# Kernel tuning notes

Hardware: AMD Instinct MI355X
Metric: run time of the kernel (lower is better)

The kernel has to match this reference:

```python
import jax, jax.numpy as jnp
import numpy as np

B, S, N_IN, N_OUT = 4, 192, 256, 1

def setup_inputs() -> dict:
    key = jax.random.key(0)
    ks = jax.random.split(key, 7)
    scale = 1.0 / np.sqrt(N_IN)
    return {
        "h_head": jax.random.normal(ks[0], (B, S, N_IN), jnp.float32),
        "h_dep": jax.random.normal(ks[1], (B, S, N_IN), jnp.float32),
        "h_sib": jax.random.normal(ks[2], (B, S, N_IN), jnp.float32),
        "W_tri": jax.random.normal(ks[3], (N_OUT, N_IN, N_IN, N_IN), jnp.float32) * (scale / N_IN),
        "U_hd": jax.random.normal(ks[4], (N_OUT, N_IN, N_IN), jnp.float32) * scale,
        "V_hs": jax.random.normal(ks[5], (N_OUT, N_IN, N_IN), jnp.float32) * scale,
        "Z_ds": jax.random.normal(ks[6], (N_OUT, N_IN, N_IN), jnp.float32) * scale,
        "bias": jnp.zeros((N_OUT,), jnp.float32),
    }

def reference(h_head, h_dep, h_sib, W_tri, U_hd, V_hs, Z_ds, bias):
    # biaffine terms: [b, x, y, o]
    s_hd = jnp.einsum('bhi,oij,bdj->bhdo', h_head, U_hd, h_dep)
    s_hs = jnp.einsum('bhi,oij,bsj->bhso', h_head, V_hs, h_sib)
    s_ds = jnp.einsum('bdi,oij,bsj->bdso', h_dep, Z_ds, h_sib)
    # trilinear term: note j,k of W_tri appear nowhere else, so they are
    # reduced first (w_red[o,i] = sum_{j,k} W_tri[o,i,j,k]) — same math as
    # torch.einsum('bhi,bdi,bsi,oijk->bhdso', ...).
    w_red = jnp.sum(W_tri, axis=(2, 3))  # [o, i]
    s_tri = jnp.einsum('bhi,bdi,bsi,oi->bhdso', h_head, h_dep, h_sib, w_red)
    scores = (s_tri
              + s_hd[:, :, :, None, :]   # unsqueeze sib axis
              + s_hs[:, :, None, :, :]   # unsqueeze dep axis
              + s_ds[:, None, :, :, :]   # unsqueeze head axis
              + bias)
    return scores[..., 0]  # n_out == 1 -> squeeze last dim
```

## Files before the change

kernel.cpp:

```cpp
#include <hip/hip_runtime.h>
#include <stdint.h>

#define NB 4
#define SS 192
#define NI 256

typedef __attribute__((ext_vector_type(8))) short bf16x8;
typedef __attribute__((ext_vector_type(16))) float f32x16;

__device__ __forceinline__ uint16_t f2bf(float f) {
  union { float f; uint32_t u; } v; v.f = f;
  return (uint16_t)((v.u + 0x7FFFu + ((v.u >> 16) & 1u)) >> 16);
}

__device__ __forceinline__ uint4 pack8(const float4 a, const float4 b) {
  uint4 r;
  r.x = (uint32_t)f2bf(a.x) | ((uint32_t)f2bf(a.y) << 16);
  r.y = (uint32_t)f2bf(a.z) | ((uint32_t)f2bf(a.w) << 16);
  r.z = (uint32_t)f2bf(b.x) | ((uint32_t)f2bf(b.y) << 16);
  r.w = (uint32_t)f2bf(b.z) | ((uint32_t)f2bf(b.w) << 16);
  return r;
}

__device__ __forceinline__ uint32_t bfmul2(uint32_t x, uint32_t y) {
  union { float f; uint32_t u; } xa, xb, ya, yb, r0, r1;
  xa.u = x << 16;        ya.u = y << 16;
  xb.u = x & 0xFFFF0000u; yb.u = y & 0xFFFF0000u;
  r0.f = xa.f * ya.f;
  r1.f = xb.f * yb.f;
  uint32_t lo = (r0.u + 0x7FFFu + ((r0.u >> 16) & 1u)) >> 16;
  uint32_t hi = (r1.u + 0x7FFFu + ((r1.u >> 16) & 1u)) >> 16;
  return lo | (hi << 16);
}


__global__ __launch_bounds__(256) void kA(
    const float* __restrict__ W,
    const float* __restrict__ h_head, const float* __restrict__ h_dep, const float* __restrict__ h_sib,
    const float* __restrict__ U, const float* __restrict__ V, const float* __restrict__ Z,
    float* __restrict__ partial,
    uint16_t* __restrict__ HH, uint16_t* __restrict__ HD, uint16_t* __restrict__ HS,
    uint16_t* __restrict__ dU16, uint16_t* __restrict__ T216, uint16_t* __restrict__ TZ16) {
  const int bi = blockIdx.x, tid = threadIdx.x;

  if (bi >= 120) {
    __shared__ float red[4];
    const int c = bi - 120;
    const float4* pw = (const float4*)(W + (size_t)c * 8192);
    float4 a = {0.f, 0.f, 0.f, 0.f};
    #pragma unroll
    for (int it = 0; it < 8; ++it) {
      const float4 v = pw[it * 256 + tid];
      a.x += v.x; a.y += v.y; a.z += v.z; a.w += v.w;
    }
    float s = (a.x + a.y) + (a.z + a.w);
    for (int off = 32; off > 0; off >>= 1) s += __shfl_down(s, off, 64);
    if ((tid & 63) == 0) red[tid >> 6] = s;
    __syncthreads();
    if (tid == 0) partial[c] = red[0] + red[1] + red[2] + red[3];
    return;
  }
  if (bi >= 24) {
    const int rl = tid >> 5, c8 = tid & 31;
    const int g = (bi - 24) * 8 + rl;
    const int dst = g * 32 + (c8 ^ (g & 15));
    const int srci = g * 64 + c8 * 2;
    { const float4 x = ((const float4*)h_head)[srci], y = ((const float4*)h_head)[srci + 1];
      ((uint4*)HH)[dst] = pack8(x, y); }
    { const float4 x = ((const float4*)h_dep)[srci], y = ((const float4*)h_dep)[srci + 1];
      ((uint4*)HD)[dst] = pack8(x, y); }
    { const float4 x = ((const float4*)h_sib)[srci], y = ((const float4*)h_sib)[srci + 1];
      ((uint4*)HS)[dst] = pack8(x, y); }
    return;
  }

  {
    __shared__ __align__(16) uint16_t Ah[192 * 128];
    __shared__ __align__(16) uint16_t Bh[128 * 128];
    const int which = bi >> 3, rem = bi & 7;
    const int b = rem >> 1, nt = rem & 1;
    const float* As = (which == 0) ? h_dep : h_sib;
    const float* Bs = (which == 0) ? U : (which == 1) ? V : Z;
    uint16_t* Os = (which == 0) ? dU16 : (which == 1) ? T216 : TZ16;
    const int lane = tid & 63, w = tid >> 6;
    const int l31 = lane & 31, l5 = lane >> 5;
    const int N0 = nt * 128;
    f32x16 acc[6] = {};

    #pragma unroll
    for (int kh = 0; kh < 2; ++kh) {
      const int kbase = kh * 128;
      if (kh) __syncthreads();
      #pragma unroll
      for (int i = 0; i < 12; ++i) {
        const int slot = i * 256 + tid;
        const int row = slot >> 4, ck = slot & 15;
        const float* sp = As + (size_t)(b * SS + row) * NI + kbase + ck * 8;
        const float4 x = *(const float4*)sp, y = *(const float4*)(sp + 4);
        *(uint4*)((char*)Ah + row * 256 + ((ck ^ (row & 15)) << 4)) = pack8(x, y);
      }
      #pragma unroll
      for (int i = 0; i < 8; ++i) {
        const int slot = i * 256 + tid;
        const int row = slot >> 4, ck = slot & 15;
        const float* sp = Bs + (size_t)(N0 + row) * NI + kbase + ck * 8;
        const float4 x = *(const float4*)sp, y = *(const float4*)(sp + 4);
        *(uint4*)((char*)Bh + row * 256 + ((ck ^ (row & 15)) << 4)) = pack8(x, y);
      }
      __syncthreads();
      const int brow = w * 32 + l31;
      const int bbyte = brow * 256;
      const int bmask = brow & 15;
      #pragma unroll
      for (int ks = 0; ks < 8; ++ks) {
        const int sl = ks * 2 + l5;
        bf16x8 bf = *reinterpret_cast<const bf16x8*>((const char*)Bh + bbyte + ((sl ^ bmask) << 4));
        #pragma unroll
        for (int mt = 0; mt < 6; ++mt) {
          const int ar = mt * 32 + l31;
          bf16x8 af = *reinterpret_cast<const bf16x8*>((const char*)Ah + ar * 256 + ((sl ^ (ar & 15)) << 4));
          acc[mt] = __builtin_amdgcn_mfma_f32_32x32x16_bf16(af, bf, acc[mt], 0, 0, 0);
        }
      }
    }
    const int n = N0 + w * 32 + l31;
    const int nck = n >> 3, npos = n & 7;
    #pragma unroll
    for (int mt = 0; mt < 6; ++mt) {
      #pragma unroll
      for (int r = 0; r < 16; ++r) {
        const int m = mt * 32 + (r & 3) + 8 * (r >> 2) + 4 * l5;
        Os[(size_t)(b * SS + m) * NI + ((nck ^ (m & 15)) << 3) + npos] = f2bf(acc[mt][r]);
      }
    }
  }
}

__global__ __launch_bounds__(384, 1) void k_s2(
    const uint16_t* __restrict__ HH, const uint16_t* __restrict__ HD,
    const uint16_t* __restrict__ dU16, const uint16_t* __restrict__ T216, const uint16_t* __restrict__ TZ16,
    float* __restrict__ s_hd, float* __restrict__ s_hs, float* __restrict__ s_ds) {
  __shared__ __align__(16) uint16_t Ah[192 * 128];
  __shared__ __align__(16) uint16_t Bh[192 * 128];
  const int which = blockIdx.x, b = blockIdx.y;
  const uint16_t* As = (which == 2) ? HD : HH;
  const uint16_t* Bs = (which == 0) ? dU16 : (which == 1) ? T216 : TZ16;
  float* Os = (which == 0) ? s_hd : (which == 1) ? s_hs : s_ds;
  const int tid = threadIdx.x, lane = tid & 63, w = tid >> 6;
  const int l31 = lane & 31, l5 = lane >> 5;
  f32x16 acc[6] = {};

  #pragma unroll
  for (int kh = 0; kh < 2; ++kh) {
    const int kbase = kh * 128;
    if (kh) __syncthreads();
    #pragma unroll
    for (int i = 0; i < 8; ++i) {
      const int slot = i * 384 + tid;
      const int row = slot >> 4, ck = slot & 15;
      const uint16_t* src = As + (size_t)(b * SS + row) * NI + kbase + ck * 8;
      __builtin_amdgcn_global_load_lds((const __attribute__((address_space(1))) void*)src,
          (__attribute__((address_space(3))) void*)(Ah + (size_t)slot * 8), 16, 0, 0);
    }
    #pragma unroll
    for (int i = 0; i < 8; ++i) {
      const int slot = i * 384 + tid;
      const int row = slot >> 4, ck = slot & 15;
      const uint16_t* src = Bs + (size_t)(b * SS + row) * NI + kbase + ck * 8;
      __builtin_amdgcn_global_load_lds((const __attribute__((address_space(1))) void*)src,
          (__attribute__((address_space(3))) void*)(Bh + (size_t)slot * 8), 16, 0, 0);
    }
    __syncthreads();
    const int brow = w * 32 + l31;
    const int bbyte = brow * 256;
    const int bmask = brow & 15;
    #pragma unroll
    for (int ks = 0; ks < 8; ++ks) {
      const int sl = ks * 2 + l5;
      bf16x8 bf = *reinterpret_cast<const bf16x8*>((const char*)Bh + bbyte + ((sl ^ bmask) << 4));
      #pragma unroll
      for (int mt = 0; mt < 6; ++mt) {
        const int ar = mt * 32 + l31;
        bf16x8 af = *reinterpret_cast<const bf16x8*>((const char*)Ah + ar * 256 + ((sl ^ (ar & 15)) << 4));
        acc[mt] = __builtin_amdgcn_mfma_f32_32x32x16_bf16(af, bf, acc[mt], 0, 0, 0);
      }
    }
  }
  const int n = w * 32 + l31;
  #pragma unroll
  for (int mt = 0; mt < 6; ++mt) {
    #pragma unroll
    for (int r = 0; r < 16; ++r) {
      const int m = mt * 32 + (r & 3) + 8 * (r >> 2) + 4 * l5;
      Os[(size_t)(b * SS + m) * SS + n] = acc[mt][r];
    }
  }
}

__global__ __launch_bounds__(576) void k3_big(
    const uint16_t* __restrict__ HH, const uint16_t* __restrict__ HS,
    const float* __restrict__ h_dep, const float* __restrict__ partial,
    const float* __restrict__ s_hd, const float* __restrict__ s_hs,
    const float* __restrict__ s_ds,
    const float* __restrict__ bias, float* __restrict__ out) {
  __shared__ __align__(16) uint16_t Btile[96 * 128];
  __shared__ __align__(16) uint16_t Atile[96 * 128];
  __shared__ uint16_t cvec[NI];
  __shared__ float chd_s[96];
  const int d = blockIdx.x, hb = blockIdx.y >> 1, sb = blockIdx.y & 1, b = blockIdx.z;
  const int tid = threadIdx.x;
  const int lane = tid & 63, w = tid >> 6;
  const int wh = w / 3, ws = w % 3;
  const int l31 = lane & 31, l5 = lane >> 5;

  if (tid < NI) {
    float wr = 0.f;
    #pragma unroll
    for (int q = 0; q < 8; ++q) wr += partial[8 * tid + q];
    cvec[tid] = f2bf(wr * h_dep[(b * SS + d) * NI + tid]);
  } else if (tid < NI + 96) {
    const int t = tid - NI;
    chd_s[t] = s_hd[(size_t)(b * SS + hb * 96 + t) * SS + d];
  }
  __syncthreads();

  f32x16 acc = {};

  #pragma unroll
  for (int half = 0; half < 2; ++half) {
    const int kbase = half * 128;
    if (half) __syncthreads();
    #pragma unroll
    for (int i = 0; i < 3; ++i) {
      const int slot = i * 576 + tid;
      if (slot < 1536) {
        const int row = slot >> 4;
        const uint16_t* src = HS + ((size_t)(b * SS + sb * 96 + row) << 8) + kbase + (slot & 15) * 8;
        __builtin_amdgcn_global_load_lds(
            (const __attribute__((address_space(1))) void*)src,
            (__attribute__((address_space(3))) void*)(Btile + (size_t)slot * 8),
            16, 0, 0);
      }
    }
    #pragma unroll
    for (int i = 0; i < 3; ++i) {
      const int slot = i * 576 + tid;
      if (slot < 1536) {
        const int row = slot >> 4;
        const int kc = slot & 15;
        const int lcl = kc ^ (row & 15);
        const uint4 cv4 = *(const uint4*)(cvec + kbase + lcl * 8);
        const uint4 hh4 = *(const uint4*)(HH + ((size_t)(b * SS + hb * 96 + row) << 8) + kbase + kc * 8);
        uint4 a4;
        a4.x = bfmul2(hh4.x, cv4.x);
        a4.y = bfmul2(hh4.y, cv4.y);
        a4.z = bfmul2(hh4.z, cv4.z);
        a4.w = bfmul2(hh4.w, cv4.w);
        *(uint4*)((char*)Atile + (size_t)slot * 16) = a4;
      }
    }
    __syncthreads();
    const int arow = wh * 32 + l31;
    const int abyte = arow * 256;
    const int amask = arow & 15;
    const int brow = ws * 32 + l31;
    const int bbyte = brow * 256;
    const int bmask = brow & 15;
    #pragma unroll
    for (int ks = 0; ks < 8; ++ks) {
      const int sl = ks * 2 + l5;
      bf16x8 af = *reinterpret_cast<const bf16x8*>((const char*)Atile + abyte + ((sl ^ amask) << 4));
      bf16x8 bf = *reinterpret_cast<const bf16x8*>((const char*)Btile + bbyte + ((sl ^ bmask) << 4));
      acc = __builtin_amdgcn_mfma_f32_32x32x16_bf16(af, bf, acc, 0, 0, 0);
    }
  }

  const float bias0 = bias[0];
  const int s = sb * 96 + ws * 32 + l31;
  const float dsv = s_ds[(b * SS + d) * SS + s];
  #pragma unroll
  for (int r = 0; r < 16; ++r) {
    const int hl = wh * 32 + (r & 3) + 8 * (r >> 2) + 4 * l5;
    const float v = acc[r] + chd_s[hl] + bias0
                  + s_hs[(size_t)(b * SS + hb * 96 + hl) * SS + s] + dsv;
    out[((size_t)(b * SS + hb * 96 + hl) * SS + d) * SS + s] = v;
  }
}

extern "C" void kernel_launch(void* const* d_in, const int* in_sizes, int n_in,
                              void* d_out, int out_size, void* d_ws, size_t ws_size,
                              hipStream_t stream) {
  const float* h_head = (const float*)d_in[0];
  const float* h_dep  = (const float*)d_in[1];
  const float* h_sib  = (const float*)d_in[2];
  const float* W_tri  = (const float*)d_in[3];
  const float* U_hd   = (const float*)d_in[4];
  const float* V_hs   = (const float*)d_in[5];
  const float* Z_ds   = (const float*)d_in[6];
  const float* bias   = (const float*)d_in[7];
  float* out = (float*)d_out;

  float* ws = (float*)d_ws;
  float* partial = ws;          ws += 2048;
  float* s_hd    = ws;          ws += NB * SS * SS;
  float* s_hs    = ws;          ws += NB * SS * SS;
  float* s_ds    = ws;          ws += NB * SS * SS;
  uint16_t* HH   = (uint16_t*)ws;
  uint16_t* HD   = HH + NB * SS * NI;
  uint16_t* HS   = HD + NB * SS * NI;
  uint16_t* dU16 = HS + NB * SS * NI;
  uint16_t* T216 = dU16 + NB * SS * NI;
  uint16_t* TZ16 = T216 + NB * SS * NI;

  kA<<<2168, 256, 0, stream>>>(W_tri, h_head, h_dep, h_sib, U_hd, V_hs, Z_ds,
                               partial, HH, HD, HS, dU16, T216, TZ16);
  k_s2<<<dim3(3, NB), 384, 0, stream>>>(HH, HD, dU16, T216, TZ16, s_hd, s_hs, s_ds);
  k3_big<<<dim3(SS, 4, NB), 576, 0, stream>>>(HH, HS, h_dep, partial,
                                              s_hd, s_hs, s_ds, bias, out);
}
```

Measured before the change: 71.29 us.

## Widen k3_big tile to cover all sib positions per block

Each k3_big block now covers 96 head rows by all 192 sib positions with 384 threads, instead of 96x96 with 576 threads. Each wave holds three accumulators and reuses one A fragment across three MFMAs. The scaled A tile (head times cvec) is therefore built once per block, removing the duplicate construction across the two sib halves, and the grid has half as many blocks. In exchange the B tile doubles, raising LDS per block to roughly 72KB, which may cut how many blocks fit on a CU, and register pressure rises from the extra accumulators.

Result: slower. 73.61 us (+3.3%).

```diff
diff --git a/kernel.cpp b/kernel.cpp
--- a/kernel.cpp
+++ b/kernel.cpp
@@ -197,20 +197,21 @@
   }
 }
 
-__global__ __launch_bounds__(576) void k3_big(
+__global__ __launch_bounds__(384, 3) void k3_big(
     const uint16_t* __restrict__ HH, const uint16_t* __restrict__ HS,
     const float* __restrict__ h_dep, const float* __restrict__ partial,
     const float* __restrict__ s_hd, const float* __restrict__ s_hs,
     const float* __restrict__ s_ds,
     const float* __restrict__ bias, float* __restrict__ out) {
-  __shared__ __align__(16) uint16_t Btile[96 * 128];
+  __shared__ __align__(16) uint16_t Btile[SS * 128];
   __shared__ __align__(16) uint16_t Atile[96 * 128];
   __shared__ uint16_t cvec[NI];
   __shared__ float chd_s[96];
-  const int d = blockIdx.x, hb = blockIdx.y >> 1, sb = blockIdx.y & 1, b = blockIdx.z;
+  const int d = blockIdx.x, hb = blockIdx.y, b = blockIdx.z;
   const int tid = threadIdx.x;
   const int lane = tid & 63, w = tid >> 6;
-  const int wh = w / 3, ws = w % 3;
+  const int whb = (w >> 1) * 32;
+  const int wsb = (w & 1) * 96;
   const int l31 = lane & 31, l5 = lane >> 5;
 
   if (tid < NI) {
@@ -224,66 +225,76 @@
   }
   __syncthreads();
 
-  f32x16 acc = {};
+  f32x16 acc0 = {}, acc1 = {}, acc2 = {};
 
   #pragma unroll
   for (int half = 0; half < 2; ++half) {
     const int kbase = half * 128;
-    if (half) __syncthreads();
-    #pragma unroll
-    for (int i = 0; i < 3; ++i) {
-      const int slot = i * 576 + tid;
-      if (slot < 1536) {
-        const int row = slot >> 4;
-        const uint16_t* src = HS + ((size_t)(b * SS + sb * 96 + row) << 8) + kbase + (slot & 15) * 8;
-        __builtin_amdgcn_global_load_lds(
-            (const __attribute__((address_space(1))) void*)src,
-            (__attribute__((address_space(3))) void*)(Btile + (size_t)slot * 8),
-            16, 0, 0);
-      }
-    }
-    #pragma unroll
-    for (int i = 0; i < 3; ++i) {
-      const int slot = i * 576 + tid;
-      if (slot < 1536) {
-        const int row = slot >> 4;
-        const int kc = slot & 15;
-        const int lcl = kc ^ (row & 15);
-        const uint4 cv4 = *(const uint4*)(cvec + kbase + lcl * 8);
-        const uint4 hh4 = *(const uint4*)(HH + ((size_t)(b * SS + hb * 96 + row) << 8) + kbase + kc * 8);
-        uint4 a4;
-        a4.x = bfmul2(hh4.x, cv4.x);
-        a4.y = bfmul2(hh4.y, cv4.y);
-        a4.z = bfmul2(hh4.z, cv4.z);
-        a4.w = bfmul2(hh4.w, cv4.w);
-        *(uint4*)((char*)Atile + (size_t)slot * 16) = a4;
-      }
+    #pragma unroll
+    for (int i = 0; i < 8; ++i) {
+      const int slot = (w * 8 + i) * 64 + lane;
+      const int row = slot >> 4;
+      const uint16_t* src = HS + ((size_t)(b * SS + row) << 8) + kbase + (slot & 15) * 8;
+      __builtin_amdgcn_global_load_lds(
+          (const __attribute__((address_space(1))) void*)src,
+          (__attribute__((address_space(3))) void*)(Btile + (size_t)slot * 8),
+          16, 0, 0);
+    }
+    #pragma unroll
+    for (int i = 0; i < 4; ++i) {
+      const int c = i * 384 + tid;
+      const int row = c >> 4;
+      const int kc = c & 15;
+      const int lcl = kc ^ (row & 15);
+      const uint4 cv4 = *(const uint4*)(cvec + kbase + lcl * 8);
+      const uint4 hh4 = *(const uint4*)(HH + ((size_t)(b * SS + hb * 96 + row) << 8) + kbase + kc * 8);
+      uint4 a4;
+      a4.x = bfmul2(hh4.x, cv4.x);
+      a4.y = bfmul2(hh4.y, cv4.y);
+      a4.z = bfmul2(hh4.z, cv4.z);
+      a4.w = bfmul2(hh4.w, cv4.w);
+      *(uint4*)((char*)Atile + row * 256 + (kc << 4)) = a4;
     }
     __syncthreads();
-    const int arow = wh * 32 + l31;
+    const int arow = whb + l31;
     const int abyte = arow * 256;
-    const int amask = arow & 15;
-    const int brow = ws * 32 + l31;
-    const int bbyte = brow * 256;
-    const int bmask = brow & 15;
+    const int amask = (arow & 15);
     #pragma unroll
     for (int ks = 0; ks < 8; ++ks) {
       const int sl = ks * 2 + l5;
       bf16x8 af = *reinterpret_cast<const bf16x8*>((const char*)Atile + abyte + ((sl ^ amask) << 4));
-      bf16x8 bf = *reinterpret_cast<const bf16x8*>((const char*)Btile + bbyte + ((sl ^ bmask) << 4));
-      acc = __builtin_amdgcn_mfma_f32_32x32x16_bf16(af, bf, acc, 0, 0, 0);
-    }
+      {
+        const int brow = wsb + l31;
+        bf16x8 bf = *reinterpret_cast<const bf16x8*>((const char*)Btile + brow * 256 + ((sl ^ (brow & 15)) << 4));
+        acc0 = __builtin_amdgcn_mfma_f32_32x32x16_bf16(af, bf, acc0, 0, 0, 0);
+      }
+      {
+        const int brow = wsb + 32 + l31;
+        bf16x8 bf = *reinterpret_cast<const bf16x8*>((const char*)Btile + brow * 256 + ((sl ^ (brow & 15)) << 4));
+        acc1 = __builtin_amdgcn_mfma_f32_32x32x16_bf16(af, bf, acc1, 0, 0, 0);
+      }
+      {
+        const int brow = wsb + 64 + l31;
+        bf16x8 bf = *reinterpret_cast<const bf16x8*>((const char*)Btile + brow * 256 + ((sl ^ (brow & 15)) << 4));
+        acc2 = __builtin_amdgcn_mfma_f32_32x32x16_bf16(af, bf, acc2, 0, 0, 0);
+      }
+    }
+    __syncthreads();
   }
 
   const float bias0 = bias[0];
-  const int s = sb * 96 + ws * 32 + l31;
-  const float dsv = s_ds[(b * SS + d) * SS + s];
   #pragma unroll
-  for (int r = 0; r < 16; ++r) {
-    const int hl = wh * 32 + (r & 3) + 8 * (r >> 2) + 4 * l5;
-    const float v = acc[r] + chd_s[hl] + bias0
-                  + s_hs[(size_t)(b * SS + hb * 96 + hl) * SS + s] + dsv;
-    out[((size_t)(b * SS + hb * 96 + hl) * SS + d) * SS + s] = v;
+  for (int t = 0; t < 3; ++t) {
+    const int s = wsb + t * 32 + l31;
+    const float dsv = s_ds[(b * SS + d) * SS + s];
+    const f32x16 a = (t == 0) ? acc0 : (t == 1) ? acc1 : acc2;
+    #pragma unroll
+    for (int r = 0; r < 16; ++r) {
+      const int hl = whb + (r & 3) + 8 * (r >> 2) + 4 * l5;
+      const float v = a[r] + chd_s[hl] + bias0
+                    + s_hs[(size_t)(b * SS + hb * 96 + hl) * SS + s] + dsv;
+      out[((size_t)(b * SS + hb * 96 + hl) * SS + d) * SS + s] = v;
+    }
   }
 }
 
@@ -315,6 +326,6 @@
   kA<<<2168, 256, 0, stream>>>(W_tri, h_head, h_dep, h_sib, U_hd, V_hs, Z_ds,
                                partial, HH, HD, HS, dU16, T216, TZ16);
   k_s2<<<dim3(3, NB), 384, 0, stream>>>(HH, HD, dU16, T216, TZ16, s_hd, s_hs, s_ds);
-  k3_big<<<dim3(SS, 4, NB), 576, 0, stream>>>(HH, HS, h_dep, partial,
+  k3_big<<<dim3(SS, 2, NB), 384, 0, stream>>>(HH, HS, h_dep, partial,
                                               s_hd, s_hs, s_ds, bias, out);
 }
```

## Fuse both biaffine GEMM stages into the prep kernel via LDS

Applied to the files above, without the earlier changes.

Merges the two biaffine GEMM stages into a single kernel. Each block now computes A·W fully (all 256 output columns) and keeps the intermediate in LDS as bf16 before doing the second GEMM, which removes the separate k_s2 launch and the global round-trip of the intermediates. Block size grows to 512 with 144KB of LDS, and the W reduction uses half as many blocks with twice the work each. The cost is much less parallelism: only 12 blocks handle the GEMMs, serialized with two GEMMs per block and 2 of 8 waves idle in the second stage.

Result: slower. 73.54 us (+3.2%).

```diff
diff --git a/kernel.cpp b/kernel.cpp
--- a/kernel.cpp
+++ b/kernel.cpp
@@ -34,141 +34,82 @@
 }
 
 
-__global__ __launch_bounds__(256) void kA(
+__global__ __launch_bounds__(512) void kA(
     const float* __restrict__ W,
     const float* __restrict__ h_head, const float* __restrict__ h_dep, const float* __restrict__ h_sib,
     const float* __restrict__ U, const float* __restrict__ V, const float* __restrict__ Z,
     float* __restrict__ partial,
-    uint16_t* __restrict__ HH, uint16_t* __restrict__ HD, uint16_t* __restrict__ HS,
-    uint16_t* __restrict__ dU16, uint16_t* __restrict__ T216, uint16_t* __restrict__ TZ16) {
+    uint16_t* __restrict__ HH, uint16_t* __restrict__ HS,
+    float* __restrict__ s_hd, float* __restrict__ s_hs, float* __restrict__ s_ds) {
   const int bi = blockIdx.x, tid = threadIdx.x;
 
-  if (bi >= 120) {
-    __shared__ float red[4];
-    const int c = bi - 120;
-    const float4* pw = (const float4*)(W + (size_t)c * 8192);
+  if (bi >= 60) {
+    __shared__ float red[8];
+    const int c = bi - 60;
+    const float4* pw = (const float4*)(W + (size_t)c * 16384);
     float4 a = {0.f, 0.f, 0.f, 0.f};
     #pragma unroll
     for (int it = 0; it < 8; ++it) {
-      const float4 v = pw[it * 256 + tid];
+      const float4 v = pw[it * 512 + tid];
       a.x += v.x; a.y += v.y; a.z += v.z; a.w += v.w;
     }
     float s = (a.x + a.y) + (a.z + a.w);
     for (int off = 32; off > 0; off >>= 1) s += __shfl_down(s, off, 64);
     if ((tid & 63) == 0) red[tid >> 6] = s;
     __syncthreads();
-    if (tid == 0) partial[c] = red[0] + red[1] + red[2] + red[3];
+    if (tid == 0) {
+      float t = 0.f;
+      #pragma unroll
+      for (int q = 0; q < 8; ++q) t += red[q];
+      partial[c] = t;
+    }
     return;
   }
-  if (bi >= 24) {
+  if (bi >= 12) {
     const int rl = tid >> 5, c8 = tid & 31;
-    const int g = (bi - 24) * 8 + rl;
+    const int g = (bi - 12) * 16 + rl;
     const int dst = g * 32 + (c8 ^ (g & 15));
     const int srci = g * 64 + c8 * 2;
     { const float4 x = ((const float4*)h_head)[srci], y = ((const float4*)h_head)[srci + 1];
       ((uint4*)HH)[dst] = pack8(x, y); }
-    { const float4 x = ((const float4*)h_dep)[srci], y = ((const float4*)h_dep)[srci + 1];
-      ((uint4*)HD)[dst] = pack8(x, y); }
     { const float4 x = ((const float4*)h_sib)[srci], y = ((const float4*)h_sib)[srci + 1];
       ((uint4*)HS)[dst] = pack8(x, y); }
     return;
   }
 
-  {
-    __shared__ __align__(16) uint16_t Ah[192 * 128];
-    __shared__ __align__(16) uint16_t Bh[128 * 128];
-    const int which = bi >> 3, rem = bi & 7;
-    const int b = rem >> 1, nt = rem & 1;
-    const float* As = (which == 0) ? h_dep : h_sib;
-    const float* Bs = (which == 0) ? U : (which == 1) ? V : Z;
-    uint16_t* Os = (which == 0) ? dU16 : (which == 1) ? T216 : TZ16;
-    const int lane = tid & 63, w = tid >> 6;
-    const int l31 = lane & 31, l5 = lane >> 5;
-    const int N0 = nt * 128;
-    f32x16 acc[6] = {};
-
-    #pragma unroll
-    for (int kh = 0; kh < 2; ++kh) {
-      const int kbase = kh * 128;
-      if (kh) __syncthreads();
-      #pragma unroll
-      for (int i = 0; i < 12; ++i) {
-        const int slot = i * 256 + tid;
-        const int row = slot >> 4, ck = slot & 15;
-        const float* sp = As + (size_t)(b * SS + row) * NI + kbase + ck * 8;
-        const float4 x = *(const float4*)sp, y = *(const float4*)(sp + 4);
-        *(uint4*)((char*)Ah + row * 256 + ((ck ^ (row & 15)) << 4)) = pack8(x, y);
-      }
-      #pragma unroll
-      for (int i = 0; i < 8; ++i) {
-        const int slot = i * 256 + tid;
-        const int row = slot >> 4, ck = slot & 15;
-        const float* sp = Bs + (size_t)(N0 + row) * NI + kbase + ck * 8;
-        const float4 x = *(const float4*)sp, y = *(const float4*)(sp + 4);
-        *(uint4*)((char*)Bh + row * 256 + ((ck ^ (row & 15)) << 4)) = pack8(x, y);
-      }
-      __syncthreads();
-      const int brow = w * 32 + l31;
-      const int bbyte = brow * 256;
-      const int bmask = brow & 15;
-      #pragma unroll
-      for (int ks = 0; ks < 8; ++ks) {
-        const int sl = ks * 2 + l5;
-        bf16x8 bf = *reinterpret_cast<const bf16x8*>((const char*)Bh + bbyte + ((sl ^ bmask) << 4));
-        #pragma unroll
-        for (int mt = 0; mt < 6; ++mt) {
-          const int ar = mt * 32 + l31;
-          bf16x8 af = *reinterpret_cast<const bf16x8*>((const char*)Ah + ar * 256 + ((sl ^ (ar & 15)) << 4));
-          acc[mt] = __builtin_amdgcn_mfma_f32_32x32x16_bf16(af, bf, acc[mt], 0, 0, 0);
-        }
-      }
-    }
-    const int n = N0 + w * 32 + l31;
-    const int nck = n >> 3, npos = n & 7;
-    #pragma unroll
-    for (int mt = 0; mt < 6; ++mt) {
-      #pragma unroll
-      for (int r = 0; r < 16; ++r) {
-        const int m = mt * 32 + (r & 3) + 8 * (r >> 2) + 4 * l5;
-        Os[(size_t)(b * SS + m) * NI + ((nck ^ (m & 15)) << 3) + npos] = f2bf(acc[mt][r]);
-      }
-    }
-  }
-}
-
-__global__ __launch_bounds__(384, 1) void k_s2(
-    const uint16_t* __restrict__ HH, const uint16_t* __restrict__ HD,
-    const uint16_t* __restrict__ dU16, const uint16_t* __restrict__ T216, const uint16_t* __restrict__ TZ16,
-    float* __restrict__ s_hd, float* __restrict__ s_hs, float* __restrict__ s_ds) {
-  __shared__ __align__(16) uint16_t Ah[192 * 128];
-  __shared__ __align__(16) uint16_t Bh[192 * 128];
-  const int which = blockIdx.x, b = blockIdx.y;
-  const uint16_t* As = (which == 2) ? HD : HH;
-  const uint16_t* Bs = (which == 0) ? dU16 : (which == 1) ? T216 : TZ16;
+  __shared__ __align__(16) unsigned char smem[147456];
+  unsigned char* Ah1 = smem;
+  unsigned char* Bh1 = smem + 49152;
+  unsigned char* Qb  = smem;
+  unsigned char* Ah2 = smem + 98304;
+  const int which = bi >> 2, b = bi & 3;
+  const float* A1 = (which == 0) ? h_dep : h_sib;
+  const float* B1 = (which == 0) ? U : (which == 1) ? V : Z;
+  const float* A2 = (which == 2) ? h_dep : h_head;
   float* Os = (which == 0) ? s_hd : (which == 1) ? s_hs : s_ds;
-  const int tid = threadIdx.x, lane = tid & 63, w = tid >> 6;
+  const int lane = tid & 63, w = tid >> 6;
   const int l31 = lane & 31, l5 = lane >> 5;
-  f32x16 acc[6] = {};
-
+
+  f32x16 acc1[6] = {};
   #pragma unroll
   for (int kh = 0; kh < 2; ++kh) {
     const int kbase = kh * 128;
     if (kh) __syncthreads();
     #pragma unroll
+    for (int i = 0; i < 6; ++i) {
+      const int slot = i * 512 + tid;
+      const int row = slot >> 4, ck = slot & 15;
+      const float* sp = A1 + (size_t)(b * SS + row) * NI + kbase + ck * 8;
+      const float4 x = *(const float4*)sp, y = *(const float4*)(sp + 4);
+      *(uint4*)(Ah1 + row * 256 + ((ck ^ (row & 15)) << 4)) = pack8(x, y);
+    }
+    #pragma unroll
     for (int i = 0; i < 8; ++i) {
-      const int slot = i * 384 + tid;
+      const int slot = i * 512 + tid;
       const int row = slot >> 4, ck = slot & 15;
-      const uint16_t* src = As + (size_t)(b * SS + row) * NI + kbase + ck * 8;
-      __builtin_amdgcn_global_load_lds((const __attribute__((address_space(1))) void*)src,
-          (__attribute__((address_space(3))) void*)(Ah + (size_t)slot * 8), 16, 0, 0);
-    }
-    #pragma unroll
-    for (int i = 0; i < 8; ++i) {
-      const int slot = i * 384 + tid;
-      const int row = slot >> 4, ck = slot & 15;
-      const uint16_t* src = Bs + (size_t)(b * SS + row) * NI + kbase + ck * 8;
-      __builtin_amdgcn_global_load_lds((const __attribute__((address_space(1))) void*)src,
-          (__attribute__((address_space(3))) void*)(Bh + (size_t)slot * 8), 16, 0, 0);
+      const float* sp = B1 + (size_t)row * NI + kbase + ck * 8;
+      const float4 x = *(const float4*)sp, y = *(const float4*)(sp + 4);
+      *(uint4*)(Bh1 + row * 256 + ((ck ^ (row & 15)) << 4)) = pack8(x, y);
     }
     __syncthreads();
     const int brow = w * 32 + l31;
@@ -177,22 +118,73 @@
     #pragma unroll
     for (int ks = 0; ks < 8; ++ks) {
       const int sl = ks * 2 + l5;
-      bf16x8 bf = *reinterpret_cast<const bf16x8*>((const char*)Bh + bbyte + ((sl ^ bmask) << 4));
+      bf16x8 bf = *reinterpret_cast<const bf16x8*>(Bh1 + bbyte + ((sl ^ bmask) << 4));
       #pragma unroll
       for (int mt = 0; mt < 6; ++mt) {
         const int ar = mt * 32 + l31;
-        bf16x8 af = *reinterpret_cast<const bf16x8*>((const char*)Ah + ar * 256 + ((sl ^ (ar & 15)) << 4));
-        acc[mt] = __builtin_amdgcn_mfma_f32_32x32x16_bf16(af, bf, acc[mt], 0, 0, 0);
-      }
-    }
-  }
-  const int n = w * 32 + l31;
+        bf16x8 af = *reinterpret_cast<const bf16x8*>(Ah1 + ar * 256 + ((sl ^ (ar & 15)) << 4));
+        acc1[mt] = __builtin_amdgcn_mfma_f32_32x32x16_bf16(af, bf, acc1[mt], 0, 0, 0);
+      }
+    }
+  }
+  __syncthreads();
+
+  {
+    const int i = w * 32 + l31;
+    unsigned char* Qh = Qb + (w >> 2) * 49152;
+    const int ic = i & 127, ck = ic >> 3, pos = i & 7;
+    #pragma unroll
+    for (int mt = 0; mt < 6; ++mt) {
+      #pragma unroll
+      for (int r = 0; r < 16; ++r) {
+        const int m = mt * 32 + (r & 3) + 8 * (r >> 2) + 4 * l5;
+        *(uint16_t*)(Qh + m * 256 + ((ck ^ (m & 15)) << 4) + pos * 2) = f2bf(acc1[mt][r]);
+      }
+    }
+  }
+  __syncthreads();
+
+  f32x16 acc2[6] = {};
   #pragma unroll
-  for (int mt = 0; mt < 6; ++mt) {
-    #pragma unroll
-    for (int r = 0; r < 16; ++r) {
-      const int m = mt * 32 + (r & 3) + 8 * (r >> 2) + 4 * l5;
-      Os[(size_t)(b * SS + m) * SS + n] = acc[mt][r];
+  for (int kh = 0; kh < 2; ++kh) {
+    const int kbase = kh * 128;
+    if (kh) __syncthreads();
+    #pragma unroll
+    for (int i = 0; i < 6; ++i) {
+      const int slot = i * 512 + tid;
+      const int row = slot >> 4, ck = slot & 15;
+      const float* sp = A2 + (size_t)(b * SS + row) * NI + kbase + ck * 8;
+      const float4 x = *(const float4*)sp, y = *(const float4*)(sp + 4);
+      *(uint4*)(Ah2 + row * 256 + ((ck ^ (row & 15)) << 4)) = pack8(x, y);
+    }
+    __syncthreads();
+    if (w < 6) {
+      const unsigned char* Qh = Qb + kh * 49152;
+      const int brow = w * 32 + l31;
+      const int bbyte = brow * 256;
+      const int bmask = brow & 15;
+      #pragma unroll
+      for (int ks = 0; ks < 8; ++ks) {
+        const int sl = ks * 2 + l5;
+        bf16x8 bf = *reinterpret_cast<const bf16x8*>(Qh + bbyte + ((sl ^ bmask) << 4));
+        #pragma unroll
+        for (int mt = 0; mt < 6; ++mt) {
+          const int ar = mt * 32 + l31;
+          bf16x8 af = *reinterpret_cast<const bf16x8*>(Ah2 + ar * 256 + ((sl ^ (ar & 15)) << 4));
+          acc2[mt] = __builtin_amdgcn_mfma_f32_32x32x16_bf16(af, bf, acc2[mt], 0, 0, 0);
+        }
+      }
+    }
+  }
+  if (w < 6) {
+    const int n = w * 32 + l31;
+    #pragma unroll
+    for (int mt = 0; mt < 6; ++mt) {
+      #pragma unroll
+      for (int r = 0; r < 16; ++r) {
+        const int m = mt * 32 + (r & 3) + 8 * (r >> 2) + 4 * l5;
+        Os[(size_t)(b * SS + m) * SS + n] = acc2[mt][r];
+      }
     }
   }
 }
@@ -214,9 +206,8 @@
   const int l31 = lane & 31, l5 = lane >> 5;
 
   if (tid < NI) {
-    float wr = 0.f;
-    #pragma unroll
-    for (int q = 0; q < 8; ++q) wr += partial[8 * tid + q];
+    const float wr = partial[4 * tid] + partial[4 * tid + 1]
+                   + partial[4 * tid + 2] + partial[4 * tid + 3];
     cvec[tid] = f2bf(wr * h_dep[(b * SS + d) * NI + tid]);
   } else if (tid < NI + 96) {
     const int t = tid - NI;
@@ -301,20 +292,15 @@
   float* out = (float*)d_out;
 
   float* ws = (float*)d_ws;
-  float* partial = ws;          ws += 2048;
+  float* partial = ws;          ws += 1024;
   float* s_hd    = ws;          ws += NB * SS * SS;
   float* s_hs    = ws;          ws += NB * SS * SS;
   float* s_ds    = ws;          ws += NB * SS * SS;
   uint16_t* HH   = (uint16_t*)ws;
-  uint16_t* HD   = HH + NB * SS * NI;
-  uint16_t* HS   = HD + NB * SS * NI;
-  uint16_t* dU16 = HS + NB * SS * NI;
-  uint16_t* T216 = dU16 + NB * SS * NI;
-  uint16_t* TZ16 = T216 + NB * SS * NI;
-
-  kA<<<2168, 256, 0, stream>>>(W_tri, h_head, h_dep, h_sib, U_hd, V_hs, Z_ds,
-                               partial, HH, HD, HS, dU16, T216, TZ16);
-  k_s2<<<dim3(3, NB), 384, 0, stream>>>(HH, HD, dU16, T216, TZ16, s_hd, s_hs, s_ds);
+  uint16_t* HS   = HH + NB * SS * NI;
+
+  kA<<<1084, 512, 0, stream>>>(W_tri, h_head, h_dep, h_sib, U_hd, V_hs, Z_ds,
+                               partial, HH, HS, s_hd, s_hs, s_ds);
   k3_big<<<dim3(SS, 4, NB), 576, 0, stream>>>(HH, HS, h_dep, partial,
                                               s_hd, s_hs, s_ds, bias, out);
 }
```
